# Optimization experiments

Measured on AMD Instinct MI355X. Metric: run time of the kernel, lower is better.

## Reference

```python
import jax, jax.numpy as jnp
import numpy as np

EPS = 1e-5  # torch LayerNorm default

def layernorm(x, gamma, beta):
    mu = jnp.mean(x, axis=-1, keepdims=True)
    var = jnp.mean(jnp.square(x - mu), axis=-1, keepdims=True)
    return (x - mu) * jax.lax.rsqrt(var + EPS) * gamma + beta

def setup_inputs() -> dict:
    key = jax.random.key(0)
    ks = jax.random.split(key, 8)
    B, S, D = 4, 2048, 1024
    s = 1.0 / np.sqrt(D)  # torch Linear init scale
    return {
        "x": jax.random.normal(ks[0], (B, S, D), dtype=jnp.float32),
        "Wq": jax.random.uniform(ks[1], (D, D), jnp.float32, -s, s),
        "bq": jax.random.uniform(ks[2], (D,), jnp.float32, -s, s),
        "Wk": jax.random.uniform(ks[3], (D, D), jnp.float32, -s, s),
        "bk": jax.random.uniform(ks[4], (D,), jnp.float32, -s, s),
        "Wv": jax.random.uniform(ks[5], (D, D), jnp.float32, -s, s),
        "bv": jax.random.uniform(ks[6], (D,), jnp.float32, -s, s),
        "gamma": jnp.ones((D,), jnp.float32),
        "beta": jnp.zeros((D,), jnp.float32),
    }

def reference(x, Wq, bq, Wk, bk, Wv, bv, gamma, beta):
    # torch Linear: x @ W.T + b; shared LayerNorm applied to each projection
    q = layernorm(jnp.einsum('bsd,ed->bse', x, Wq) + bq, gamma, beta)
    k = layernorm(jnp.einsum('bsd,ed->bse', x, Wk) + bk, gamma, beta)
    v = layernorm(jnp.einsum('bsd,ed->bse', x, Wv) + bv, gamma, beta)
    att = jnp.einsum('bqd,bkd->bqk', q, k)  # no 1/sqrt(d) scaling in original
    att = jax.nn.softmax(att, axis=-1)
    # dropout is identity in eval mode (reference baseline)
    return jnp.einsum('bqk,bkd->bqd', att, v)
```

## Files before the change

kernel.cpp:

```cpp
#include <hip/hip_runtime.h>

typedef _Float16 f16;
typedef __attribute__((ext_vector_type(4))) _Float16 f16x4;
typedef __attribute__((ext_vector_type(8))) _Float16 f16x8;
typedef __attribute__((ext_vector_type(4))) float f32x4;

#define GLB_AS __attribute__((address_space(1)))
#define LDS_AS __attribute__((address_space(3)))

__device__ __forceinline__ void async_copy16(const void* g, void* l) {
  __builtin_amdgcn_global_load_lds((const GLB_AS void*)g, (LDS_AS void*)l, 16, 0, 0);
}

#define WAITVM(N) asm volatile("s_waitcnt vmcnt(" #N ")" ::: "memory")
#define WAITLGKM0() asm volatile("s_waitcnt lgkmcnt(0)" ::: "memory")
#define BAR() __builtin_amdgcn_s_barrier()
#define SB0() __builtin_amdgcn_sched_barrier(0)

template <typename OutT, int MODE, bool BIAS>
__global__ __launch_bounds__(256, 4) void gemm_kn(
    const f16* __restrict__ A, const f16* __restrict__ B, OutT* __restrict__ C,
    int lda, int ldb, int ldc, int K, long sA, long sB, long sC,
    int tiles_x, int tiles_y,
    const float* __restrict__ b0, const float* __restrict__ b1,
    const float* __restrict__ b2)
{
  constexpr int BM = 128, BK = 32;
  __shared__ __align__(16) f16 Ash[2][BM * BK];
  __shared__ __align__(16) f16 Bsh[2][BM * BK];

  int bx, by, bz;
  {
    const int n = blockIdx.x;
    if (MODE == 0) {
      by = n % tiles_y;
      const int r = n / tiles_y;
      bx = r % tiles_x;
      bz = r / tiles_x;
    } else {
      const int j = n & 7, i = n >> 3;
      bz = j >> 1;
      bx = i >> 3;
      by = (j & 1) * 8 + (i & 7);
    }
  }

  A += (long)bz * sA;
  B += (long)bz * sB;
  C += (long)bz * sC;

  const int tid  = threadIdx.x;
  const int wave = tid >> 6, lane = tid & 63;
  const int m0 = by * BM, n0 = bx * BM;
  const int wm = (wave >> 1) * 64, wn = (wave & 1) * 64;
  const int r16 = lane & 15, quad = lane >> 4;

  const int srow = wave * 32 + (lane >> 2);
  const int skb  = ((lane & 3) ^ ((lane >> 3) & 3)) * 8;
  const f16* Ag = A + (long)(m0 + srow) * lda + skb;
  const f16* Bg = B + (long)(n0 + srow) * ldb + skb;
  const int lo0 = (wave * 32) * BK;
  const int lo1 = (wave * 32 + 16) * BK;

  async_copy16(Ag,                  &Ash[0][lo0]);
  async_copy16(Ag + 16 * (long)lda, &Ash[0][lo1]);
  async_copy16(Bg,                  &Bsh[0][lo0]);
  async_copy16(Bg + 16 * (long)ldb, &Bsh[0][lo1]);

  f32x4 acc[4][4] = {};

  const int cchunk = (quad ^ ((r16 >> 1) & 3)) * 8;

  int buf = 0;
  for (int k0 = 0; k0 < K; k0 += BK, buf ^= 1) {
    __syncthreads();

    if (k0 + BK < K) {
      const int nb = buf ^ 1;
      const long k1 = k0 + BK;
      async_copy16(Ag + k1,                  &Ash[nb][lo0]);
      async_copy16(Ag + k1 + 16 * (long)lda, &Ash[nb][lo1]);
      async_copy16(Bg + k1,                  &Bsh[nb][lo0]);
      async_copy16(Bg + k1 + 16 * (long)ldb, &Bsh[nb][lo1]);
    }

    f16x8 bf[4];
#pragma unroll
    for (int j = 0; j < 4; j++)
      bf[j] = *(const f16x8*)&Bsh[buf][(wn + j * 16 + r16) * BK + cchunk];
#pragma unroll
    for (int i = 0; i < 4; i++) {
      f16x8 af = *(const f16x8*)&Ash[buf][(wm + i * 16 + r16) * BK + cchunk];
#pragma unroll
      for (int j = 0; j < 4; j++)
        acc[i][j] = __builtin_amdgcn_mfma_f32_16x16x32_f16(af, bf[j], acc[i][j], 0, 0, 0);
    }
  }

  float bias_j[4] = {0.f, 0.f, 0.f, 0.f};
  if (BIAS) {
    const float* bias = (bz == 0) ? b0 : (bz == 1) ? b1 : b2;
#pragma unroll
    for (int j = 0; j < 4; j++) bias_j[j] = bias[n0 + wn + j * 16 + r16];
  }
#pragma unroll
  for (int i = 0; i < 4; i++)
#pragma unroll
    for (int j = 0; j < 4; j++)
#pragma unroll
      for (int r = 0; r < 4; r++) {
        long row = m0 + wm + i * 16 + quad * 4 + r;
        long col = n0 + wn + j * 16 + r16;
        C[row * (long)ldc + col] = (OutT)(acc[i][j][r] + bias_j[j]);
      }
}

#define STAGE_A(t_, kk_) do {                                                \
    const long _k = (long)(t_) * 64 + (kk_) * 32;                            \
    f16* _d = &Ash[(t_) & 1][kk_][w16 * 32];                                 \
    async_copy16(Ag + _k, _d);                                               \
    if constexpr (IA == 2) async_copy16(Ag + _k + 128l * lda, _d + 4096);    \
  } while (0)
#define STAGE_B(t_, kk_) do {                                                \
    const long _k = (long)(t_) * 64 + (kk_) * 32;                            \
    f16* _d = &Bsh[(t_) & 1][kk_][w16 * 32];                                 \
    async_copy16(Bg + _k, _d);                                               \
    async_copy16(Bg + _k + 128l * ldb, _d + 4096);                           \
  } while (0)

template <int BM, int BN, typename OutT, int MODE, bool BIAS>
__global__ __launch_bounds__(512, 2) void gemm8p(
    const f16* __restrict__ A, const f16* __restrict__ B, OutT* __restrict__ C,
    int lda, int ldb, int ldc, int K, long sA, long sB, long sC,
    int tiles_x, int tiles_y,
    const float* __restrict__ b0, const float* __restrict__ b1,
    const float* __restrict__ b2)
{
  constexpr int WM = BM / 2, WN = BN / 4;
  constexpr int RM = WM / 16, RN = WN / 16;
  constexpr int IA = BM / 128;
  static_assert(RN == 4 && BN == 256, "template assumes BN=256");

  __shared__ __align__(16) f16 Ash[2][2][BM * 32];
  __shared__ __align__(16) f16 Bsh[2][2][BN * 32];

  int bx, by, bz;
  {
    const int n = blockIdx.x;
    if (MODE == 0) {
      by = n % tiles_y;
      const int r = n / tiles_y;
      bx = r % tiles_x;
      bz = r / tiles_x;
    } else {
      const int j = n & 7, i = n >> 3, th = tiles_y >> 1;
      bz = j >> 1;
      bx = i / th;
      by = (j & 1) * th + i % th;
    }
  }

  A += (long)bz * sA;
  B += (long)bz * sB;
  C += (long)bz * sC;

  const int tid  = threadIdx.x;
  const int wave = tid >> 6, lane = tid & 63;
  const int wr = wave >> 2, wc = wave & 3;
  const int m0 = by * BM, n0 = bx * BN;
  const int r16 = lane & 15, quad = lane >> 4;
  const int w16 = wave * 16;

  const int cg8 = (((lane & 3) ^ ((lane >> 2) & 3) ^ ((lane >> 4) & 3)) * 8);
  const f16* Ag = A + (long)(m0 + w16 + (lane >> 2)) * lda + cg8;
  const f16* Bg = B + (long)(n0 + w16 + (lane >> 2)) * ldb + cg8;

  const int NT = K / 64;

  STAGE_A(0, 0); STAGE_B(0, 0);
  STAGE_A(0, 1); STAGE_B(0, 1);
  STAGE_A(1, 0); STAGE_B(1, 0);

  f32x4 acc[RM][RN] = {};

  const int rc  = (quad ^ ((r16 ^ (r16 >> 2)) & 3)) * 8;
  const int rdA = (wr * WM + r16) * 32 + rc;
  const int rdB = (wc * WN + r16) * 32 + rc;

  if constexpr (RM == 8) { WAITVM(8); } else { WAITVM(6); }
  BAR();

  for (int t = 0; t < NT; ++t) {
    const int bp = t & 1;
    const f16* A0 = &Ash[bp][0][0];
    const f16* A1 = &Ash[bp][1][0];
    const f16* B0 = &Bsh[bp][0][0];
    const f16* B1 = &Bsh[bp][1][0];
    f16x8 af[4], bf[4];

    if constexpr (RM == 4) {
#pragma unroll
      for (int i = 0; i < 4; i++) af[i] = *(const f16x8*)&A0[rdA + i * 512];
#pragma unroll
      for (int j = 0; j < 4; j++) bf[j] = *(const f16x8*)&B0[rdB + j * 512];
      if (t + 1 < NT) { STAGE_A(t + 1, 1); STAGE_B(t + 1, 1); }
      BAR();
      WAITLGKM0(); SB0();
      __builtin_amdgcn_s_setprio(1);
#pragma unroll
      for (int i = 0; i < 4; i++)
#pragma unroll
        for (int j = 0; j < 4; j++)
          acc[i][j] = __builtin_amdgcn_mfma_f32_16x16x32_f16(af[i], bf[j], acc[i][j], 0, 0, 0);
      __builtin_amdgcn_s_setprio(0); SB0();
      if (t < NT - 1) { WAITVM(6); } else { WAITVM(0); }
      BAR();
#pragma unroll
      for (int i = 0; i < 4; i++) af[i] = *(const f16x8*)&A1[rdA + i * 512];
#pragma unroll
      for (int j = 0; j < 4; j++) bf[j] = *(const f16x8*)&B1[rdB + j * 512];
      if (t + 2 < NT) { STAGE_A(t + 2, 0); STAGE_B(t + 2, 0); }
      BAR();
      WAITLGKM0(); SB0();
      __builtin_amdgcn_s_setprio(1);
#pragma unroll
      for (int i = 0; i < 4; i++)
#pragma unroll
        for (int j = 0; j < 4; j++)
          acc[i][j] = __builtin_amdgcn_mfma_f32_16x16x32_f16(af[i], bf[j], acc[i][j], 0, 0, 0);
      __builtin_amdgcn_s_setprio(0); SB0();
      if (t < NT - 2) { WAITVM(6); } else if (t == NT - 2) { WAITVM(3); } else { WAITVM(0); }
      BAR();
    } else {
#pragma unroll
      for (int i = 0; i < 4; i++) af[i] = *(const f16x8*)&A0[rdA + i * 512];
#pragma unroll
      for (int j = 0; j < 4; j++) bf[j] = *(const f16x8*)&B0[rdB + j * 512];
      if (t + 1 < NT) STAGE_A(t + 1, 1);
      BAR();
      WAITLGKM0(); SB0();
      __builtin_amdgcn_s_setprio(1);
#pragma unroll
      for (int i = 0; i < 4; i++)
#pragma unroll
        for (int j = 0; j < 4; j++)
          acc[i][j] = __builtin_amdgcn_mfma_f32_16x16x32_f16(af[i], bf[j], acc[i][j], 0, 0, 0);
      __builtin_amdgcn_s_setprio(0); SB0();
      BAR();
#pragma unroll
      for (int i = 0; i < 4; i++) af[i] = *(const f16x8*)&A0[rdA + (4 + i) * 512];
      if (t + 1 < NT) STAGE_B(t + 1, 1);
      BAR();
      WAITLGKM0(); SB0();
      __builtin_amdgcn_s_setprio(1);
#pragma unroll
      for (int i = 0; i < 4; i++)
#pragma unroll
        for (int j = 0; j < 4; j++)
          acc[4 + i][j] = __builtin_amdgcn_mfma_f32_16x16x32_f16(af[i], bf[j], acc[4 + i][j], 0, 0, 0);
      __builtin_amdgcn_s_setprio(0); SB0();
      if (t < NT - 1) { WAITVM(6); } else { WAITVM(0); }
      BAR();
#pragma unroll
      for (int i = 0; i < 4; i++) af[i] = *(const f16x8*)&A1[rdA + i * 512];
#pragma unroll
      for (int j = 0; j < 4; j++) bf[j] = *(const f16x8*)&B1[rdB + j * 512];
      if (t + 2 < NT) STAGE_A(t + 2, 0);
      BAR();
      WAITLGKM0(); SB0();
      __builtin_amdgcn_s_setprio(1);
#pragma unroll
      for (int i = 0; i < 4; i++)
#pragma unroll
        for (int j = 0; j < 4; j++)
          acc[i][j] = __builtin_amdgcn_mfma_f32_16x16x32_f16(af[i], bf[j], acc[i][j], 0, 0, 0);
      __builtin_amdgcn_s_setprio(0); SB0();
      BAR();
#pragma unroll
      for (int i = 0; i < 4; i++) af[i] = *(const f16x8*)&A1[rdA + (4 + i) * 512];
      if (t + 2 < NT) STAGE_B(t + 2, 0);
      BAR();
      WAITLGKM0(); SB0();
      __builtin_amdgcn_s_setprio(1);
#pragma unroll
      for (int i = 0; i < 4; i++)
#pragma unroll
        for (int j = 0; j < 4; j++)
          acc[4 + i][j] = __builtin_amdgcn_mfma_f32_16x16x32_f16(af[i], bf[j], acc[4 + i][j], 0, 0, 0);
      __builtin_amdgcn_s_setprio(0); SB0();
      if (t < NT - 2) { WAITVM(6); } else if (t == NT - 2) { WAITVM(4); } else { WAITVM(0); }
      BAR();
    }
  }

  float bias_j[RN];
#pragma unroll
  for (int j = 0; j < RN; j++) bias_j[j] = 0.f;
  if constexpr (BIAS) {
    const float* bias = (bz == 0) ? b0 : (bz == 1) ? b1 : b2;
#pragma unroll
    for (int j = 0; j < RN; j++) bias_j[j] = bias[n0 + wc * WN + j * 16 + r16];
  }
#pragma unroll
  for (int i = 0; i < RM; i++)
#pragma unroll
    for (int j = 0; j < RN; j++)
#pragma unroll
      for (int r = 0; r < 4; r++) {
        long row = m0 + wr * WM + i * 16 + quad * 4 + r;
        long col = n0 + wc * WN + j * 16 + r16;
        C[row * (long)ldc + col] = (OutT)(acc[i][j][r] + bias_j[j]);
      }
}

__global__ __launch_bounds__(256) void cast_all(
    const float* __restrict__ x, const float* __restrict__ Wq,
    const float* __restrict__ Wk, const float* __restrict__ Wv,
    f16* __restrict__ Xh, f16* __restrict__ Wh)
{
  const long off = (long)blockIdx.x * 1024 + threadIdx.x * 4;
  const float* src;
  f16* dst;
  if (off < 8388608L) {
    src = x + off;
    dst = Xh + off;
  } else {
    const long o = off - 8388608L;
    src = (o < 1048576L) ? Wq + o
        : (o < 2097152L) ? Wk + (o - 1048576L)
                         : Wv + (o - 2097152L);
    dst = Wh + o;
  }
  const float4 v = *(const float4*)src;
  f16x4 h;
  h.x = (f16)v.x; h.y = (f16)v.y; h.z = (f16)v.z; h.w = (f16)v.w;
  *(f16x4*)dst = h;
}

__global__ __launch_bounds__(256) void ln_kernel(
    f16* __restrict__ P, const float* __restrict__ gamma,
    const float* __restrict__ beta)
{
  f16* p = P + (long)blockIdx.y * 8388608 + (long)blockIdx.x * 1024;
  const int tid = threadIdx.x;
  const int e = tid * 4;

  f16x4 raw = *(const f16x4*)(p + e);
  float v0 = (float)raw.x, v1 = (float)raw.y;
  float v2 = (float)raw.z, v3 = (float)raw.w;
  float s  = v0 + v1 + v2 + v3;
  float s2 = v0 * v0 + v1 * v1 + v2 * v2 + v3 * v3;

#pragma unroll
  for (int off = 32; off > 0; off >>= 1) {
    s  += __shfl_down(s, off, 64);
    s2 += __shfl_down(s2, off, 64);
  }
  __shared__ float red[10];
  const int wave = tid >> 6, lane = tid & 63;
  if (lane == 0) { red[wave] = s; red[4 + wave] = s2; }
  __syncthreads();
  if (tid == 0) {
    red[8] = red[0] + red[1] + red[2] + red[3];
    red[9] = red[4] + red[5] + red[6] + red[7];
  }
  __syncthreads();
  const float mu   = red[8] * (1.f / 1024.f);
  const float var  = red[9] * (1.f / 1024.f) - mu * mu;
  const float rstd = rsqrtf(var + 1e-5f);

  float4 gg = *(const float4*)(gamma + e);
  float4 be = *(const float4*)(beta + e);
  f16x4 o;
  o.x = (f16)((v0 - mu) * rstd * gg.x + be.x);
  o.y = (f16)((v1 - mu) * rstd * gg.y + be.y);
  o.z = (f16)((v2 - mu) * rstd * gg.z + be.z);
  o.w = (f16)((v3 - mu) * rstd * gg.w + be.w);
  *(f16x4*)(p + e) = o;
}

__global__ __launch_bounds__(256) void transpose_kernel(const f16* __restrict__ V,
                                                        f16* __restrict__ Vt)
{
  const int S = 2048, D = 1024;
  const f16* v = V + (long)blockIdx.z * ((long)S * D);
  f16* vt = Vt + (long)blockIdx.z * ((long)D * S);
  __shared__ f16 tile[64][66];
  const int d0 = blockIdx.x * 64, j0 = blockIdx.y * 64;
  const int tx = threadIdx.x & 63, ty = threadIdx.x >> 6;
#pragma unroll
  for (int r = ty; r < 64; r += 4)
    tile[r][tx] = v[(long)(j0 + r) * D + d0 + tx];
  __syncthreads();
#pragma unroll
  for (int r = ty; r < 64; r += 4)
    vt[(long)(d0 + r) * S + j0 + tx] = tile[tx][r];
}

__global__ __launch_bounds__(256) void softmax_kernel(float* __restrict__ Sc)
{
  float* srow = Sc + (long)blockIdx.x * 2048;
  const int tid = threadIdx.x;
  float4 a = ((const float4*)srow)[tid];
  float4 b = ((const float4*)srow)[256 + tid];

  float m = fmaxf(fmaxf(fmaxf(a.x, a.y), fmaxf(a.z, a.w)),
                  fmaxf(fmaxf(b.x, b.y), fmaxf(b.z, b.w)));
#pragma unroll
  for (int off = 32; off > 0; off >>= 1) m = fmaxf(m, __shfl_down(m, off, 64));
  __shared__ float red[6];
  const int wave = tid >> 6, lane = tid & 63;
  if (lane == 0) red[wave] = m;
  __syncthreads();
  if (tid == 0) red[4] = fmaxf(fmaxf(red[0], red[1]), fmaxf(red[2], red[3]));
  __syncthreads();
  const float M = red[4];

  a.x = __expf(a.x - M); a.y = __expf(a.y - M);
  a.z = __expf(a.z - M); a.w = __expf(a.w - M);
  b.x = __expf(b.x - M); b.y = __expf(b.y - M);
  b.z = __expf(b.z - M); b.w = __expf(b.w - M);
  float s = a.x + a.y + a.z + a.w + b.x + b.y + b.z + b.w;
#pragma unroll
  for (int off = 32; off > 0; off >>= 1) s += __shfl_down(s, off, 64);
  if (lane == 0) red[wave] = s;
  __syncthreads();
  if (tid == 0) red[5] = red[0] + red[1] + red[2] + red[3];
  __syncthreads();
  const float inv = 1.0f / red[5];

  f16* orow = (f16*)srow;
  f16x4 oa, ob;
  oa.x = (f16)(a.x * inv); oa.y = (f16)(a.y * inv);
  oa.z = (f16)(a.z * inv); oa.w = (f16)(a.w * inv);
  ob.x = (f16)(b.x * inv); ob.y = (f16)(b.y * inv);
  ob.z = (f16)(b.z * inv); ob.w = (f16)(b.w * inv);
  ((f16x4*)orow)[tid]       = oa;
  ((f16x4*)orow)[256 + tid] = ob;
}

extern "C" void kernel_launch(void* const* d_in, const int* in_sizes, int n_in,
                              void* d_out, int out_size, void* d_ws, size_t ws_size,
                              hipStream_t stream)
{
  const float* x     = (const float*)d_in[0];
  const float* Wq    = (const float*)d_in[1];
  const float* bq    = (const float*)d_in[2];
  const float* Wk    = (const float*)d_in[3];
  const float* bk    = (const float*)d_in[4];
  const float* Wv    = (const float*)d_in[5];
  const float* bv    = (const float*)d_in[6];
  const float* gamma = (const float*)d_in[7];
  const float* beta  = (const float*)d_in[8];
  float* out = (float*)d_out;

  char* ws = (char*)d_ws;
  f16*   P  = (f16*)(ws);
  f16*   Vt = (f16*)(ws + (48u << 20));
  float* Sc = (float*)(ws + (64u << 20));
  f16*   Xh = (f16*)(ws + (64u << 20));
  f16*   Wh = (f16*)(ws + (80u << 20));

  cast_all<<<11264, 256, 0, stream>>>(x, Wq, Wk, Wv, Xh, Wh);

  gemm_kn<f16, 0, true><<<1536, 256, 0, stream>>>(
      Xh, Wh, P, 1024, 1024, 1024, 1024, 0L, 1048576L, 8388608L,
      8, 64, bq, bk, bv);

  ln_kernel<<<dim3(8192, 3), 256, 0, stream>>>(P, gamma, beta);

  transpose_kernel<<<dim3(16, 32, 4), 256, 0, stream>>>(P + 2L * 8388608, Vt);

  gemm8p<256, 256, float, 1, false><<<256, 512, 0, stream>>>(
      P, P + 8388608, Sc, 1024, 1024, 2048, 1024, 2097152L, 2097152L, 4194304L,
      8, 8, nullptr, nullptr, nullptr);

  softmax_kernel<<<8192, 256, 0, stream>>>(Sc);

  gemm8p<128, 256, float, 1, false><<<256, 512, 0, stream>>>(
      (const f16*)Sc, Vt, out, 4096, 2048, 1024, 2048, 8388608L, 2097152L, 2097152L,
      4, 16, nullptr, nullptr, nullptr);
}
```

Before: 300.7 us.

## Fuse tile-local softmax into QK GEMM epilogue with per-tile rescale in PV GEMM

The QK^T GEMM now computes per-tile row max and exp-sum in its epilogue and writes unnormalized fp16 exponentials plus tile statistics instead of fp32 scores. A small kernel merges the eight column-tile statistics per row into rescale factors, which the PV GEMM applies to its A fragments on load. This drops the standalone softmax pass and halves the score-matrix write and read traffic. In exchange it adds LDS reductions in the epilogue, a tiny extra launch, and fp16 multiplies in the PV inner loop. The rescale factors are also rounded to fp16, which costs precision.

```diff
diff --git a/kernel.cpp b/kernel.cpp
--- a/kernel.cpp
+++ b/kernel.cpp
@@ -128,13 +128,14 @@
     async_copy16(Bg + _k + 128l * ldb, _d + 4096);                           \
   } while (0)
 
-template <int BM, int BN, typename OutT, int MODE, bool BIAS>
+template <int BM, int BN, typename OutT, int MODE, bool BIAS, int EPI, bool ALPHA>
 __global__ __launch_bounds__(512, 2) void gemm8p(
     const f16* __restrict__ A, const f16* __restrict__ B, OutT* __restrict__ C,
     int lda, int ldb, int ldc, int K, long sA, long sB, long sC,
     int tiles_x, int tiles_y,
     const float* __restrict__ b0, const float* __restrict__ b1,
-    const float* __restrict__ b2)
+    const float* __restrict__ b2,
+    float2* __restrict__ statsB, const float* __restrict__ alphaB)
 {
   constexpr int WM = BM / 2, WN = BN / 4;
   constexpr int RM = WM / 16, RN = WN / 16;
@@ -187,10 +188,22 @@
   const int rdA = (wr * WM + r16) * 32 + rc;
   const int rdB = (wc * WN + r16) * 32 + rc;
 
+  f16 ah[RM == 4 ? 4 : 1];
+  const float* aBase = nullptr;
+  if constexpr (ALPHA) aBase = alphaB + (long)bz * 8 * 2048 + m0 + wr * WM + r16;
+
   if constexpr (RM == 8) { WAITVM(8); } else { WAITVM(6); }
   BAR();
 
   for (int t = 0; t < NT; ++t) {
+    if constexpr (ALPHA) {
+      if ((t & 3) == 0) {
+        const int T = t >> 2;
+#pragma unroll
+        for (int i = 0; i < 4; i++)
+          ah[i] = (f16)aBase[(long)T * 2048 + i * 16];
+      }
+    }
     const int bp = t & 1;
     const f16* A0 = &Ash[bp][0][0];
     const f16* A1 = &Ash[bp][1][0];
@@ -200,7 +213,10 @@
 
     if constexpr (RM == 4) {
 #pragma unroll
-      for (int i = 0; i < 4; i++) af[i] = *(const f16x8*)&A0[rdA + i * 512];
+      for (int i = 0; i < 4; i++) {
+        af[i] = *(const f16x8*)&A0[rdA + i * 512];
+        if constexpr (ALPHA) af[i] = af[i] * ah[i];
+      }
 #pragma unroll
       for (int j = 0; j < 4; j++) bf[j] = *(const f16x8*)&B0[rdB + j * 512];
       if (t + 1 < NT) { STAGE_A(t + 1, 1); STAGE_B(t + 1, 1); }
@@ -216,7 +232,10 @@
       if (t < NT - 1) { WAITVM(6); } else { WAITVM(0); }
       BAR();
 #pragma unroll
-      for (int i = 0; i < 4; i++) af[i] = *(const f16x8*)&A1[rdA + i * 512];
+      for (int i = 0; i < 4; i++) {
+        af[i] = *(const f16x8*)&A1[rdA + i * 512];
+        if constexpr (ALPHA) af[i] = af[i] * ah[i];
+      }
 #pragma unroll
       for (int j = 0; j < 4; j++) bf[j] = *(const f16x8*)&B1[rdB + j * 512];
       if (t + 2 < NT) { STAGE_A(t + 2, 0); STAGE_B(t + 2, 0); }
@@ -293,6 +312,62 @@
     }
   }
 
+  if constexpr (EPI == 1) {
+    float* red = (float*)&Ash[0][0][0];
+    float* fin = red + 1024;
+
+    float mloc[RM][4];
+#pragma unroll
+    for (int i = 0; i < RM; i++)
+#pragma unroll
+      for (int r = 0; r < 4; r++) {
+        float m = fmaxf(fmaxf(acc[i][0][r], acc[i][1][r]),
+                        fmaxf(acc[i][2][r], acc[i][3][r]));
+#pragma unroll
+        for (int msk = 1; msk <= 8; msk <<= 1) m = fmaxf(m, __shfl_xor(m, msk, 64));
+        mloc[i][r] = m;
+      }
+    if (r16 == 0) {
+#pragma unroll
+      for (int i = 0; i < RM; i++)
+#pragma unroll
+        for (int r = 0; r < 4; r++)
+          red[(wr * 128 + i * 16 + quad * 4 + r) * 4 + wc] = mloc[i][r];
+    }
+    __syncthreads();
+    if (tid < 256)
+      fin[tid] = fmaxf(fmaxf(red[tid * 4], red[tid * 4 + 1]),
+                       fmaxf(red[tid * 4 + 2], red[tid * 4 + 3]));
+    __syncthreads();
+#pragma unroll
+    for (int i = 0; i < RM; i++)
+#pragma unroll
+      for (int r = 0; r < 4; r++) {
+        const float m = fin[wr * 128 + i * 16 + quad * 4 + r];
+        float s = 0.f;
+#pragma unroll
+        for (int j = 0; j < 4; j++) {
+          acc[i][j][r] = __expf(acc[i][j][r] - m);
+          s += acc[i][j][r];
+        }
+#pragma unroll
+        for (int msk = 1; msk <= 8; msk <<= 1) s += __shfl_xor(s, msk, 64);
+        mloc[i][r] = s;
+      }
+    if (r16 == 0) {
+#pragma unroll
+      for (int i = 0; i < RM; i++)
+#pragma unroll
+        for (int r = 0; r < 4; r++)
+          red[(wr * 128 + i * 16 + quad * 4 + r) * 4 + wc] = mloc[i][r];
+    }
+    __syncthreads();
+    if (tid < 256) {
+      const float L = red[tid * 4] + red[tid * 4 + 1] + red[tid * 4 + 2] + red[tid * 4 + 3];
+      statsB[((long)bz * 8 + bx) * 2048 + m0 + tid] = make_float2(fin[tid], L);
+    }
+  }
+
   float bias_j[RN];
 #pragma unroll
   for (int j = 0; j < RN; j++) bias_j[j] = 0.f;
@@ -311,6 +386,29 @@
         long col = n0 + wc * WN + j * 16 + r16;
         C[row * (long)ldc + col] = (OutT)(acc[i][j][r] + bias_j[j]);
       }
+}
+
+__global__ __launch_bounds__(256) void reduce_stats(
+    const float2* __restrict__ st, float* __restrict__ al)
+{
+  const int r = blockIdx.x * 256 + threadIdx.x;
+  const int bz = r >> 11, row = r & 2047;
+  float m[8], l[8];
+#pragma unroll
+  for (int t = 0; t < 8; t++) {
+    const float2 v = st[((long)bz * 8 + t) * 2048 + row];
+    m[t] = v.x; l[t] = v.y;
+  }
+  float M = m[0];
+#pragma unroll
+  for (int t = 1; t < 8; t++) M = fmaxf(M, m[t]);
+  float L = 0.f;
+#pragma unroll
+  for (int t = 0; t < 8; t++) L += l[t] * __expf(m[t] - M);
+  const float inv = 1.0f / L;
+#pragma unroll
+  for (int t = 0; t < 8; t++)
+    al[((long)bz * 8 + t) * 2048 + row] = __expf(m[t] - M) * inv;
 }
 
 __global__ __launch_bounds__(256) void cast_all(
@@ -397,48 +495,6 @@
     vt[(long)(d0 + r) * S + j0 + tx] = tile[tx][r];
 }
 
-__global__ __launch_bounds__(256) void softmax_kernel(float* __restrict__ Sc)
-{
-  float* srow = Sc + (long)blockIdx.x * 2048;
-  const int tid = threadIdx.x;
-  float4 a = ((const float4*)srow)[tid];
-  float4 b = ((const float4*)srow)[256 + tid];
-
-  float m = fmaxf(fmaxf(fmaxf(a.x, a.y), fmaxf(a.z, a.w)),
-                  fmaxf(fmaxf(b.x, b.y), fmaxf(b.z, b.w)));
-#pragma unroll
-  for (int off = 32; off > 0; off >>= 1) m = fmaxf(m, __shfl_down(m, off, 64));
-  __shared__ float red[6];
-  const int wave = tid >> 6, lane = tid & 63;
-  if (lane == 0) red[wave] = m;
-  __syncthreads();
-  if (tid == 0) red[4] = fmaxf(fmaxf(red[0], red[1]), fmaxf(red[2], red[3]));
-  __syncthreads();
-  const float M = red[4];
-
-  a.x = __expf(a.x - M); a.y = __expf(a.y - M);
-  a.z = __expf(a.z - M); a.w = __expf(a.w - M);
-  b.x = __expf(b.x - M); b.y = __expf(b.y - M);
-  b.z = __expf(b.z - M); b.w = __expf(b.w - M);
-  float s = a.x + a.y + a.z + a.w + b.x + b.y + b.z + b.w;
-#pragma unroll
-  for (int off = 32; off > 0; off >>= 1) s += __shfl_down(s, off, 64);
-  if (lane == 0) red[wave] = s;
-  __syncthreads();
-  if (tid == 0) red[5] = red[0] + red[1] + red[2] + red[3];
-  __syncthreads();
-  const float inv = 1.0f / red[5];
-
-  f16* orow = (f16*)srow;
-  f16x4 oa, ob;
-  oa.x = (f16)(a.x * inv); oa.y = (f16)(a.y * inv);
-  oa.z = (f16)(a.z * inv); oa.w = (f16)(a.w * inv);
-  ob.x = (f16)(b.x * inv); ob.y = (f16)(b.y * inv);
-  ob.z = (f16)(b.z * inv); ob.w = (f16)(b.w * inv);
-  ((f16x4*)orow)[tid]       = oa;
-  ((f16x4*)orow)[256 + tid] = ob;
-}
-
 extern "C" void kernel_launch(void* const* d_in, const int* in_sizes, int n_in,
                               void* d_out, int out_size, void* d_ws, size_t ws_size,
                               hipStream_t stream)
@@ -455,11 +511,13 @@
   float* out = (float*)d_out;
 
   char* ws = (char*)d_ws;
-  f16*   P  = (f16*)(ws);
-  f16*   Vt = (f16*)(ws + (48u << 20));
-  float* Sc = (float*)(ws + (64u << 20));
-  f16*   Xh = (f16*)(ws + (64u << 20));
-  f16*   Wh = (f16*)(ws + (80u << 20));
+  f16*    P     = (f16*)(ws);
+  f16*    Vt    = (f16*)(ws + (48u << 20));
+  f16*    Pr    = (f16*)(ws + (64u << 20));
+  f16*    Xh    = (f16*)(ws + (64u << 20));
+  f16*    Wh    = (f16*)(ws + (80u << 20));
+  float2* stats = (float2*)(ws + (96u << 20));
+  float*  alpha = (float*)(ws + (96u << 20) + (512u << 10));
 
   cast_all<<<11264, 256, 0, stream>>>(x, Wq, Wk, Wv, Xh, Wh);
 
@@ -471,13 +529,13 @@
 
   transpose_kernel<<<dim3(16, 32, 4), 256, 0, stream>>>(P + 2L * 8388608, Vt);
 
-  gemm8p<256, 256, float, 1, false><<<256, 512, 0, stream>>>(
-      P, P + 8388608, Sc, 1024, 1024, 2048, 1024, 2097152L, 2097152L, 4194304L,
-      8, 8, nullptr, nullptr, nullptr);
-
-  softmax_kernel<<<8192, 256, 0, stream>>>(Sc);
-
-  gemm8p<128, 256, float, 1, false><<<256, 512, 0, stream>>>(
-      (const f16*)Sc, Vt, out, 4096, 2048, 1024, 2048, 8388608L, 2097152L, 2097152L,
-      4, 16, nullptr, nullptr, nullptr);
-}
+  gemm8p<256, 256, f16, 1, false, 1, false><<<256, 512, 0, stream>>>(
+      P, P + 8388608, Pr, 1024, 1024, 2048, 1024, 2097152L, 2097152L, 4194304L,
+      8, 8, nullptr, nullptr, nullptr, stats, nullptr);
+
+  reduce_stats<<<32, 256, 0, stream>>>(stats, alpha);
+
+  gemm8p<128, 256, float, 1, false, 0, true><<<256, 512, 0, stream>>>(
+      Pr, Vt, out, 2048, 2048, 1024, 2048, 4194304L, 2097152L, 2097152L,
+      4, 16, nullptr, nullptr, nullptr, nullptr, alpha);
+}
```

After: 292.8 us. 2.6% less time.
